# Kernel optimization log

Hardware: AMD Instinct MI355X
Metric: run time of the kernel (lower is better)

## Reference

```python
import jax, jax.numpy as jnp
import numpy as np

B, L, D, HD, DC = 2, 2048, 2048, 64, 2048
NH = D // HD  # 32 heads


def _rms_norm(x, eps):
    return x * jax.lax.rsqrt(jnp.mean(jnp.square(x), axis=-1, keepdims=True) + eps)


def _apply_rope(x, rope):
    # x: [b,h,l,d]; rope: [2,l,d]. x_hat = interleave(-x_odd, x_even)
    x2 = x.reshape(*x.shape[:-1], HD // 2, 2)
    x_hat = jnp.stack([-x2[..., 1], x2[..., 0]], axis=-1).reshape(x.shape)
    return x * rope[0] + x_hat * rope[1]


def setup_inputs() -> dict:
    key = jax.random.key(0)
    ks = jax.random.split(key, 6)
    return {
        "x": jax.random.normal(ks[0], (B, L, D), jnp.float32),
        "condition": jax.random.normal(ks[1], (B, DC), jnp.float32),
        "rope": jax.random.normal(ks[2], (2, L, HD), jnp.float32),
        "w_ada": jax.random.normal(ks[3], (2 * D, DC), jnp.float32) * 0.02,
        "w_qkv": jax.random.normal(ks[4], (3 * D, D), jnp.float32) * 0.02,
        "w_out": jax.random.normal(ks[5], (D, D), jnp.float32) * 0.02,
        "qk_w": jnp.ones((HD,), jnp.float32),
    }


def reference(x, condition, rope, w_ada, w_qkv, w_out, qk_w):
    eps = jnp.finfo(x.dtype).eps
    # AdaRMSNorm
    ss = (condition @ w_ada.T)[:, None, :]          # [b,1,2D]
    shift, scale = jnp.split(ss, 2, axis=-1)
    h = _rms_norm(x, eps) * (1.0 + scale) + shift   # [b,l,D]
    # fused QKV projection: 'b l (n h d)'
    qkv = (h @ w_qkv.T).reshape(B, L, 3, NH, HD)
    qkv = jnp.transpose(qkv, (2, 0, 3, 1, 4))       # [3,b,h,l,d]
    q, k, v = qkv[0], qkv[1], qkv[2]
    # per-head RMSNorm (with affine weight) + RoPE
    q = _apply_rope(_rms_norm(q, eps) * qk_w, rope)
    k = _apply_rope(_rms_norm(k, eps) * qk_w, rope)
    # SDPA
    scores = jnp.einsum('bhqd,bhkd->bhqk', q, k) / jnp.sqrt(jnp.asarray(HD, x.dtype))
    attn = jax.nn.softmax(scores, axis=-1)
    o = jnp.einsum('bhqk,bhkd->bhqd', attn, v)      # [b,h,l,d]
    o = jnp.transpose(o, (0, 2, 1, 3)).reshape(B, L, D)
    return o @ w_out.T
```

## Files before the change

### kernel.cpp

```cpp
#include <hip/hip_runtime.h>


typedef __bf16 bf16x8 __attribute__((ext_vector_type(8)));
typedef float  f32x4  __attribute__((ext_vector_type(4)));
typedef float  f32x16 __attribute__((ext_vector_type(16)));

#define EPS_F32 1.1920929e-07f
#define QSCALE 0.18033688011112042f

#if defined(__has_builtin)
#  if __has_builtin(__builtin_amdgcn_exp2f)
#    define EXP2F(x) __builtin_amdgcn_exp2f(x)
#  else
#    define EXP2F(x) __expf((x) * 0.6931471805599453f)
#  endif
#  if __has_builtin(__builtin_amdgcn_rcpf)
#    define RCPF(x) __builtin_amdgcn_rcpf(x)
#  else
#    define RCPF(x) (1.0f / (x))
#  endif
#else
#  define EXP2F(x) __expf((x) * 0.6931471805599453f)
#  define RCPF(x) (1.0f / (x))
#endif

__device__ __forceinline__ float bf2f(unsigned int u16) {
  union { unsigned int i; float f; } v; v.i = (u16 & 0xffffu) << 16; return v.f;
}
__device__ __forceinline__ float bf2f_hi(unsigned int u32) {
  union { unsigned int i; float f; } v; v.i = u32 & 0xffff0000u; return v.f;
}
__device__ __forceinline__ unsigned short f2bf(float f) {
  union { float f; unsigned int i; } v; v.f = f;
  unsigned int r = v.i + 0x7fffu + ((v.i >> 16) & 1u);
  return (unsigned short)(r >> 16);
}
__device__ __forceinline__ unsigned int f2bf_rn_u(float f) {
  union { float f; unsigned int i; } v; v.f = f;
  return v.i + 0x8000u;
}

__device__ __forceinline__ void gload16(const void* g, void* l) {
  __builtin_amdgcn_global_load_lds(
      (const __attribute__((address_space(1))) unsigned int*)(unsigned long long)g,
      (__attribute__((address_space(3))) unsigned int*)(unsigned int)(unsigned long long)l,
      16, 0, 0);
}

__global__ __launch_bounds__(256) void ada_gemm_kernel(
    const float* __restrict__ cond, const float* __restrict__ w_ada,
    float* __restrict__ ss)
{
  const int lane = threadIdx.x & 63;
  const int gw = blockIdx.x * 4 + (threadIdx.x >> 6);
  const int b = gw >> 12;
  const int j = gw & 4095;
  const float4* wr = (const float4*)(w_ada + j * 2048);
  const float4* cr = (const float4*)(cond + b * 2048);
  float acc = 0.f;
  #pragma unroll
  for (int k4 = 0; k4 < 8; ++k4) {
    float4 w = wr[lane + k4 * 64];
    float4 c = cr[lane + k4 * 64];
    acc += w.x * c.x + w.y * c.y + w.z * c.z + w.w * c.w;
  }
  #pragma unroll
  for (int off = 1; off < 64; off <<= 1) acc += __shfl_xor(acc, off);
  if (lane == 0) ss[b * 4096 + j] = acc;
}

__global__ __launch_bounds__(256) void ada_rms_kernel(
    const float* __restrict__ x, const float* __restrict__ ss,
    unsigned short* __restrict__ H)
{
  const int row = blockIdx.x;
  const int b = row >> 11;
  const int tid = threadIdx.x;
  const int lane = tid & 63, wave = tid >> 6;
  const float* xr = x + (size_t)row * 2048;
  float4 v0 = ((const float4*)xr)[tid * 2];
  float4 v1 = ((const float4*)xr)[tid * 2 + 1];
  float ssq = v0.x*v0.x + v0.y*v0.y + v0.z*v0.z + v0.w*v0.w
            + v1.x*v1.x + v1.y*v1.y + v1.z*v1.z + v1.w*v1.w;
  #pragma unroll
  for (int off = 1; off < 64; off <<= 1) ssq += __shfl_xor(ssq, off);
  __shared__ float red[4];
  if (lane == 0) red[wave] = ssq;
  __syncthreads();
  const float tot = red[0] + red[1] + red[2] + red[3];
  const float r = rsqrtf(tot * (1.f / 2048.f) + EPS_F32);
  const int c0 = tid * 8;
  const float* sh = ss + b * 4096;
  float xv[8] = {v0.x, v0.y, v0.z, v0.w, v1.x, v1.y, v1.z, v1.w};
  unsigned int pk[4];
  #pragma unroll
  for (int p = 0; p < 4; ++p) {
    const int c = c0 + p * 2;
    float h0 = xv[p*2+0] * r * (1.f + sh[2048 + c])     + sh[c];
    float h1 = xv[p*2+1] * r * (1.f + sh[2048 + c + 1]) + sh[c + 1];
    pk[p] = (unsigned int)f2bf(h0) | ((unsigned int)f2bf(h1) << 16);
  }
  *(uint4*)&H[(size_t)row * 2048 + c0] = make_uint4(pk[0], pk[1], pk[2], pk[3]);
}

__global__ __launch_bounds__(256) void cast2_kernel(
    const float* __restrict__ a,
    const float* __restrict__ b,
    unsigned short* __restrict__ dst)
{
  const int i = blockIdx.x * 256 + threadIdx.x;
  float4 v = (i < 3145728) ? ((const float4*)a)[i]
                           : ((const float4*)b)[i - 3145728];
  unsigned int p0 = (unsigned int)f2bf(v.x) | ((unsigned int)f2bf(v.y) << 16);
  unsigned int p1 = (unsigned int)f2bf(v.z) | ((unsigned int)f2bf(v.w) << 16);
  *(uint2*)&dst[(size_t)i * 4] = make_uint2(p0, p1);
}

__global__ __launch_bounds__(512, 2) void gemm_qkv_8p(
    const unsigned short* __restrict__ A,
    const unsigned short* __restrict__ Bw,
    unsigned short* __restrict__ C,
    unsigned short* __restrict__ vt)
{
  __shared__ unsigned short As[2][2][8192];
  __shared__ unsigned short Bs[2][2][8192];

  const int tid  = threadIdx.x;
  const int lane = tid & 63;
  const int wave = tid >> 6;
  const int wrow = (wave >> 2) * 128;
  const int wcol = (wave & 3) * 64;

  const int swz = (blockIdx.x & 7) * 48 + (blockIdx.x >> 3);
  const int bx = swz >> 4;
  const int by = swz & 15;
  const int bm = by * 256;
  const int bn = bx * 256;

  const int fr = lane & 15;
  const int q_ = lane >> 4;
  const int laneoff = fr * 32 + ((q_ ^ ((fr >> 1) & 3)) << 3);

  const int rA  = wave * 32 + (lane >> 2);
  const int kk  = (lane & 3) ^ ((lane >> 3) & 3);
  const unsigned short* Ag0 = A  + (size_t)(bm + rA) * 2048 + kk * 8;
  const unsigned short* Ag1 = Ag0 + (size_t)16 * 2048;
  const unsigned short* Bg0 = Bw + (size_t)(bn + rA) * 2048 + kk * 8;
  const unsigned short* Bg1 = Bg0 + (size_t)16 * 2048;
  const int ldso = rA * 32 + (lane & 3) * 8;

  f32x4 acc[8][4] = {};
  bf16x8 fA[4], fB[4];

#define STAGE_A(SB, SKH, KT) do { \
    gload16(Ag0 + (KT) * 64 + (SKH) * 32, &As[SB][SKH][ldso]); \
    gload16(Ag1 + (KT) * 64 + (SKH) * 32, &As[SB][SKH][ldso + 512]); } while (0)
#define STAGE_B(SB, SKH, KT) do { \
    gload16(Bg0 + (KT) * 64 + (SKH) * 32, &Bs[SB][SKH][ldso]); \
    gload16(Bg1 + (KT) * 64 + (SKH) * 32, &Bs[SB][SKH][ldso + 512]); } while (0)
#define VMW(N) asm volatile("s_waitcnt vmcnt(" #N ")" ::: "memory")
#define LDB(BUF, KH) do { const unsigned short* p_ = &Bs[BUF][KH][wcol * 32 + laneoff]; \
    fB[0] = *(const bf16x8*)&p_[0];    fB[1] = *(const bf16x8*)&p_[512]; \
    fB[2] = *(const bf16x8*)&p_[1024]; fB[3] = *(const bf16x8*)&p_[1536]; } while (0)
#define LDA(BUF, KH, MH) do { const unsigned short* p_ = &As[BUF][KH][(wrow + (MH) * 64) * 32 + laneoff]; \
    fA[0] = *(const bf16x8*)&p_[0];    fA[1] = *(const bf16x8*)&p_[512]; \
    fA[2] = *(const bf16x8*)&p_[1024]; fA[3] = *(const bf16x8*)&p_[1536]; } while (0)
#define MFMA16(MH) do { \
    _Pragma("unroll") \
    for (int f_ = 0; f_ < 4; ++f_) { \
      _Pragma("unroll") \
      for (int n_ = 0; n_ < 4; ++n_) \
        acc[(MH) * 4 + f_][n_] = __builtin_amdgcn_mfma_f32_16x16x32_bf16( \
            fA[f_], fB[n_], acc[(MH) * 4 + f_][n_], 0, 0, 0); \
    } } while (0)
#define PH_MID() do { __builtin_amdgcn_s_barrier(); \
    asm volatile("s_waitcnt lgkmcnt(0)"); \
    __builtin_amdgcn_s_setprio(1); } while (0)
#define PH_END() do { __builtin_amdgcn_s_setprio(0); \
    __builtin_amdgcn_s_barrier(); } while (0)

  STAGE_A(0, 0, 0); STAGE_B(0, 0, 0); STAGE_A(0, 1, 0); STAGE_B(0, 1, 0);
  VMW(4);
  __builtin_amdgcn_s_barrier();

  for (int it = 0; it < 16; ++it) {
    const int t1 = 2 * it + 1;
    const int t2 = 2 * it + 2;
    const bool pf = (it < 15);

    LDB(0, 0); LDA(0, 0, 0);
    STAGE_A(1, 0, t1);
    PH_MID(); MFMA16(0); PH_END();
    LDA(0, 0, 1);
    STAGE_B(1, 0, t1);
    VMW(4);
    PH_MID(); MFMA16(1); PH_END();
    LDB(0, 1); LDA(0, 1, 0);
    STAGE_A(1, 1, t1);
    PH_MID(); MFMA16(0); PH_END();
    LDA(0, 1, 1);
    STAGE_B(1, 1, t1);
    VMW(4);
    PH_MID(); MFMA16(1); PH_END();

    LDB(1, 0); LDA(1, 0, 0);
    if (pf) STAGE_A(0, 0, t2);
    PH_MID(); MFMA16(0); PH_END();
    LDA(1, 0, 1);
    if (pf) { STAGE_B(0, 0, t2); VMW(4); }
    else    { VMW(0); }
    PH_MID(); MFMA16(1); PH_END();
    LDB(1, 1); LDA(1, 1, 0);
    if (pf) STAGE_A(0, 1, t2);
    PH_MID(); MFMA16(0); PH_END();
    LDA(1, 1, 1);
    if (pf) STAGE_B(0, 1, t2);
    VMW(4);
    PH_MID(); MFMA16(1); PH_END();
  }

#undef STAGE_A
#undef STAGE_B
#undef VMW
#undef LDB
#undef LDA
#undef MFMA16
#undef PH_MID
#undef PH_END

  const int cr = (lane >> 4) * 4;
  const int cc = lane & 15;
  if (bn >= 4096) {
    #pragma unroll
    for (int mf = 0; mf < 8; ++mf)
      #pragma unroll
      for (int nf = 0; nf < 4; ++nf)
        #pragma unroll
        for (int r = 0; r < 4; ++r) {
          const int m  = bm + wrow + mf * 16 + cr + r;
          const int dg = bn + wcol + nf * 16 + cc - 4096;
          const int l  = m & 2047;
          const size_t dst = ((size_t)((m >> 11) * 32 + (dg >> 6)) * 64 + (dg & 63)) * 2048
                           + (l >> 6) * 64 + (l & 15) * 4 + ((l >> 4) & 3);
          vt[dst] = f2bf(acc[mf][nf][r]);
        }
  } else {
    #pragma unroll
    for (int mf = 0; mf < 8; ++mf)
      #pragma unroll
      for (int nf = 0; nf < 4; ++nf)
        #pragma unroll
        for (int r = 0; r < 4; ++r) {
          const int row = bm + wrow + mf * 16 + cr + r;
          const int col = bn + wcol + nf * 16 + cc;
          C[(size_t)row * 6144 + col] = f2bf(acc[mf][nf][r]);
        }
  }
}

__global__ __launch_bounds__(512, 1) void gemm_out_4p(
    const unsigned short* __restrict__ A,
    const unsigned short* __restrict__ Bw,
    float* __restrict__ C)
{
  __shared__ unsigned short As[2][2][8192];
  __shared__ unsigned short Bs[2][2][4096];

  const int tid  = threadIdx.x;
  const int lane = tid & 63;
  const int wave = tid >> 6;
  const int wrow = (wave >> 1) * 64;
  const int wcol = (wave & 1) * 64;

  const int swz = (blockIdx.x & 7) * 32 + (blockIdx.x >> 3);
  const int bx = swz >> 4;
  const int by = swz & 15;
  const int bm = by * 256;
  const int bn = bx * 128;

  const int fr = lane & 15;
  const int q_ = lane >> 4;
  const int laneoff = fr * 32 + ((q_ ^ ((fr >> 1) & 3)) << 3);

  const int rA = wave * 32 + (lane >> 2);
  const int rB = wave * 16 + (lane >> 2);
  const int kk = (lane & 3) ^ ((lane >> 3) & 3);
  const unsigned short* Ag0 = A  + (size_t)(bm + rA) * 2048 + kk * 8;
  const unsigned short* Ag1 = Ag0 + (size_t)16 * 2048;
  const unsigned short* Bg0 = Bw + (size_t)(bn + rB) * 2048 + kk * 8;
  const int ldsoA = rA * 32 + (lane & 3) * 8;
  const int ldsoB = rB * 32 + (lane & 3) * 8;

  f32x4 acc[4][4] = {};
  bf16x8 fA[4], fB[4];

#define STAGE_A4(SB, SKH, KT) do { \
    gload16(Ag0 + (KT) * 64 + (SKH) * 32, &As[SB][SKH][ldsoA]); \
    gload16(Ag1 + (KT) * 64 + (SKH) * 32, &As[SB][SKH][ldsoA + 512]); } while (0)
#define STAGE_B4(SB, SKH, KT) \
    gload16(Bg0 + (KT) * 64 + (SKH) * 32, &Bs[SB][SKH][ldsoB])
#define VMW(N) asm volatile("s_waitcnt vmcnt(" #N ")" ::: "memory")
#define LDB4(BUF, KH) do { const unsigned short* p_ = &Bs[BUF][KH][wcol * 32 + laneoff]; \
    fB[0] = *(const bf16x8*)&p_[0];    fB[1] = *(const bf16x8*)&p_[512]; \
    fB[2] = *(const bf16x8*)&p_[1024]; fB[3] = *(const bf16x8*)&p_[1536]; } while (0)
#define LDA4(BUF, KH) do { const unsigned short* p_ = &As[BUF][KH][wrow * 32 + laneoff]; \
    fA[0] = *(const bf16x8*)&p_[0];    fA[1] = *(const bf16x8*)&p_[512]; \
    fA[2] = *(const bf16x8*)&p_[1024]; fA[3] = *(const bf16x8*)&p_[1536]; } while (0)
#define MFMA16_4() do { \
    _Pragma("unroll") \
    for (int f_ = 0; f_ < 4; ++f_) { \
      _Pragma("unroll") \
      for (int n_ = 0; n_ < 4; ++n_) \
        acc[f_][n_] = __builtin_amdgcn_mfma_f32_16x16x32_bf16( \
            fA[f_], fB[n_], acc[f_][n_], 0, 0, 0); \
    } } while (0)
#define PH_MID() do { __builtin_amdgcn_s_barrier(); \
    asm volatile("s_waitcnt lgkmcnt(0)"); \
    __builtin_amdgcn_s_setprio(1); } while (0)
#define PH_END() do { __builtin_amdgcn_s_setprio(0); \
    __builtin_amdgcn_s_barrier(); } while (0)

  STAGE_A4(0, 0, 0); STAGE_B4(0, 0, 0);
  STAGE_A4(0, 1, 0); STAGE_B4(0, 1, 0);
  VMW(3);
  __builtin_amdgcn_s_barrier();

  for (int it = 0; it < 16; ++it) {
    const int t1 = 2 * it + 1;
    const int t2 = 2 * it + 2;
    const bool pf = (it < 15);

    LDB4(0, 0); LDA4(0, 0);
    STAGE_A4(1, 0, t1); STAGE_B4(1, 0, t1);
    VMW(3);
    PH_MID(); MFMA16_4(); PH_END();
    LDB4(0, 1); LDA4(0, 1);
    STAGE_A4(1, 1, t1); STAGE_B4(1, 1, t1);
    VMW(3);
    PH_MID(); MFMA16_4(); PH_END();

    LDB4(1, 0); LDA4(1, 0);
    if (pf) { STAGE_A4(0, 0, t2); STAGE_B4(0, 0, t2); VMW(3); }
    else    { VMW(0); }
    PH_MID(); MFMA16_4(); PH_END();
    LDB4(1, 1); LDA4(1, 1);
    if (pf) { STAGE_A4(0, 1, t2); STAGE_B4(0, 1, t2); VMW(3); }
    else    { VMW(0); }
    PH_MID(); MFMA16_4(); PH_END();
  }

#undef STAGE_A4
#undef STAGE_B4
#undef VMW
#undef LDB4
#undef LDA4
#undef MFMA16_4
#undef PH_MID
#undef PH_END

  const int cr = (lane >> 4) * 4;
  const int cc = lane & 15;
  #pragma unroll
  for (int f = 0; f < 4; ++f)
    #pragma unroll
    for (int n = 0; n < 4; ++n)
      #pragma unroll
      for (int r = 0; r < 4; ++r) {
        const int row = bm + wrow + f * 16 + cr + r;
        const int col = bn + wcol + n * 16 + cc;
        C[(size_t)row * 2048 + col] = acc[f][n][r];
      }
}

__global__ __launch_bounds__(256) void qk_rope_kernel(
    unsigned short* __restrict__ QKV, const float* __restrict__ rope,
    const float* __restrict__ qk_w)
{
  const int tid  = threadIdx.x;
  const int lane = tid & 63;
  const int task = blockIdx.x * 4 + (tid >> 6);
  const int hg   = task & 3;
  const int bl   = task >> 2;
  const int l    = bl & 2047;
  const int h    = hg * 8 + (lane >> 3);
  const int d0   = (lane & 7) * 8;
  const size_t base = (size_t)bl * 6144 + h * 64 + d0;

  float r0[8], r1[8], wv[8];
  {
    const float4* p0 = (const float4*)(rope + l * 64 + d0);
    const float4* p1 = (const float4*)(rope + 131072 + l * 64 + d0);
    const float4* pw = (const float4*)(qk_w + d0);
    float4 a, b2;
    a = p0[0]; b2 = p0[1];
    r0[0]=a.x; r0[1]=a.y; r0[2]=a.z; r0[3]=a.w; r0[4]=b2.x; r0[5]=b2.y; r0[6]=b2.z; r0[7]=b2.w;
    a = p1[0]; b2 = p1[1];
    r1[0]=a.x; r1[1]=a.y; r1[2]=a.z; r1[3]=a.w; r1[4]=b2.x; r1[5]=b2.y; r1[6]=b2.z; r1[7]=b2.w;
    a = pw[0]; b2 = pw[1];
    wv[0]=a.x; wv[1]=a.y; wv[2]=a.z; wv[3]=a.w; wv[4]=b2.x; wv[5]=b2.y; wv[6]=b2.z; wv[7]=b2.w;
  }

  #pragma unroll
  for (int t = 0; t < 2; ++t) {
    unsigned short* p = &QKV[base + (size_t)2048 * t];
    const uint4 raw = *(const uint4*)p;
    const unsigned int* u = (const unsigned int*)&raw;
    float v[8];
    #pragma unroll
    for (int j = 0; j < 4; ++j) {
      v[2*j]   = bf2f(u[j]);
      v[2*j+1] = bf2f_hi(u[j]);
    }
    float sq = v[0]*v[0] + v[1]*v[1] + v[2]*v[2] + v[3]*v[3]
             + v[4]*v[4] + v[5]*v[5] + v[6]*v[6] + v[7]*v[7];
    sq += __shfl_xor(sq, 1);
    sq += __shfl_xor(sq, 2);
    sq += __shfl_xor(sq, 4);
    const float rn = rsqrtf(sq * (1.f / 64.f) + EPS_F32)
                   * ((t == 0) ? QSCALE : 1.0f);
    float vn[8];
    #pragma unroll
    for (int j = 0; j < 8; ++j) vn[j] = v[j] * (rn * wv[j]);
    unsigned int pk[4];
    #pragma unroll
    for (int j = 0; j < 4; ++j) {
      const float o0 = vn[2*j]   * r0[2*j]   - vn[2*j+1] * r1[2*j];
      const float o1 = vn[2*j+1] * r0[2*j+1] + vn[2*j]   * r1[2*j+1];
      pk[j] = (unsigned int)f2bf(o0) | ((unsigned int)f2bf(o1) << 16);
    }
    *(uint4*)p = make_uint4(pk[0], pk[1], pk[2], pk[3]);
  }
}

__global__ __launch_bounds__(256, 2) void attn_mfma_kernel(
    const unsigned short* __restrict__ QKV,
    const unsigned short* __restrict__ Vt,
    unsigned short* __restrict__ O)
{
  __shared__ unsigned short Ks[64 * 72];
  __shared__ unsigned short Vs[64 * 72];
  __shared__ unsigned short Ps[4 * 64 * 68];
  const int tid  = threadIdx.x;
  const int lane = tid & 63;
  const int wave = tid >> 6;
  const int blk = blockIdx.x;
  const int bh = blk & 63;
  const int qt = blk >> 6;
  const int b = bh >> 5, h = bh & 31;
  const int rowbase = b << 11;
  const int qbase = qt * 256 + wave * 64;

  const int m16  = lane & 15;
  const int quad = lane >> 4;
  const int m32  = lane & 31;
  const int hl   = lane >> 5;

  bf16x8 qf[4][2];
  #pragma unroll
  for (int qi = 0; qi < 4; ++qi)
    #pragma unroll
    for (int ch = 0; ch < 2; ++ch)
      qf[qi][ch] = *(const bf16x8*)&QKV[(size_t)(rowbase + qbase + qi * 16 + m16) * 6144
                                        + h * 64 + ch * 32 + quad * 8];

  const int sr = tid >> 2;
  const int sc = (tid & 3) * 16;
  const unsigned short* Kg = QKV + (size_t)(rowbase + sr) * 6144 + 2048 + h * 64 + sc;
  const unsigned short* Vg = Vt + (size_t)(bh * 64 + sr) * 2048 + sc;

  f32x16 accO[2][2] = {};
  float part[4][4] = {};
  unsigned short* Pw = &Ps[(wave * 64) * 68];

  for (int kt = 0; kt < 32; ++kt) {
    __syncthreads();
    {
      const uint4* kp = (const uint4*)(Kg + (size_t)kt * 64 * 6144);
      const uint4* vp = (const uint4*)(Vg + kt * 64);
      uint4 k0 = kp[0], k1 = kp[1];
      uint4 v0 = vp[0], v1 = vp[1];
      *(uint4*)&Ks[sr * 72 + sc]     = k0;
      *(uint4*)&Ks[sr * 72 + sc + 8] = k1;
      *(uint4*)&Vs[sr * 72 + sc]     = v0;
      *(uint4*)&Vs[sr * 72 + sc + 8] = v1;
    }
    __syncthreads();

    unsigned int pk[4][4][2];
    #pragma unroll
    for (int kj = 0; kj < 4; ++kj) {
      bf16x8 kf0 = *(const bf16x8*)&Ks[(kj * 16 + m16) * 72 + quad * 8];
      bf16x8 kf1 = *(const bf16x8*)&Ks[(kj * 16 + m16) * 72 + 32 + quad * 8];
      #pragma unroll
      for (int qi = 0; qi < 4; ++qi) {
        f32x4 acc = {};
        acc = __builtin_amdgcn_mfma_f32_16x16x32_bf16(qf[qi][0], kf0, acc, 0, 0, 0);
        acc = __builtin_amdgcn_mfma_f32_16x16x32_bf16(qf[qi][1], kf1, acc, 0, 0, 0);
        #pragma unroll
        for (int r = 0; r < 4; ++r) {
          float p = EXP2F(acc[r]);
          part[qi][r] += p;
          unsigned int pb = f2bf_rn_u(p);
          if (kj == 0)      pk[qi][r][0]  = pb >> 16;
          else if (kj == 1) pk[qi][r][0] |= pb & 0xffff0000u;
          else if (kj == 2) pk[qi][r][1]  = pb >> 16;
          else              pk[qi][r][1] |= pb & 0xffff0000u;
        }
      }
    }
    #pragma unroll
    for (int qi = 0; qi < 4; ++qi)
      #pragma unroll
      for (int r = 0; r < 4; ++r)
        *(uint2*)&Pw[(qi * 16 + quad * 4 + r) * 68 + m16 * 4] =
            make_uint2(pk[qi][r][0], pk[qi][r][1]);

    #pragma unroll
    for (int ch = 0; ch < 4; ++ch) {
      bf16x8 pa0 = *(const bf16x8*)&Pw[m32 * 68 + ch * 16 + hl * 8];
      bf16x8 pa1 = *(const bf16x8*)&Pw[(32 + m32) * 68 + ch * 16 + hl * 8];
      bf16x8 vb0 = *(const bf16x8*)&Vs[m32 * 72 + ch * 16 + hl * 8];
      bf16x8 vb1 = *(const bf16x8*)&Vs[(32 + m32) * 72 + ch * 16 + hl * 8];
      accO[0][0] = __builtin_amdgcn_mfma_f32_32x32x16_bf16(pa0, vb0, accO[0][0], 0, 0, 0);
      accO[0][1] = __builtin_amdgcn_mfma_f32_32x32x16_bf16(pa0, vb1, accO[0][1], 0, 0, 0);
      accO[1][0] = __builtin_amdgcn_mfma_f32_32x32x16_bf16(pa1, vb0, accO[1][0], 0, 0, 0);
      accO[1][1] = __builtin_amdgcn_mfma_f32_32x32x16_bf16(pa1, vb1, accO[1][1], 0, 0, 0);
    }
  }

  #pragma unroll
  for (int qi = 0; qi < 4; ++qi)
    #pragma unroll
    for (int r = 0; r < 4; ++r)
      #pragma unroll
      for (int off = 1; off < 16; off <<= 1)
        part[qi][r] += __shfl_xor(part[qi][r], off);

  #pragma unroll
  for (int qs = 0; qs < 2; ++qs) {
    #pragma unroll
    for (int reg = 0; reg < 16; ++reg) {
      const int r = reg & 3;
      const int s = reg >> 2;
      const int qsrc = ((2 * s + hl) & 3) * 16 + m16;
      const float rs = __shfl(part[qs * 2 + (reg >> 3)][r], qsrc);
      const float inv = RCPF(rs);
      const int rho = r + 8 * s + 4 * hl;
      const size_t base = (size_t)(rowbase + qbase + qs * 32 + rho) * 2048 + h * 64;
      O[base + m32]      = f2bf(accO[qs][0][reg] * inv);
      O[base + 32 + m32] = f2bf(accO[qs][1][reg] * inv);
    }
  }
}

extern "C" void kernel_launch(void* const* d_in, const int* in_sizes, int n_in,
                              void* d_out, int out_size, void* d_ws, size_t ws_size,
                              hipStream_t stream) {
  (void)in_sizes; (void)n_in; (void)out_size; (void)ws_size;
  const float* x     = (const float*)d_in[0];
  const float* cond  = (const float*)d_in[1];
  const float* rope  = (const float*)d_in[2];
  const float* w_ada = (const float*)d_in[3];
  const float* w_qkv = (const float*)d_in[4];
  const float* w_out = (const float*)d_in[5];
  const float* qk_w  = (const float*)d_in[6];
  float* out = (float*)d_out;

  char* ws = (char*)d_ws;
  float*          ss   = (float*)ws;
  unsigned short* H    = (unsigned short*)(ws + 32768);
  unsigned short* Wq   = H + 8388608;
  unsigned short* Wo   = Wq + 12582912;
  unsigned short* QKV  = Wo + 4194304;
  unsigned short* Vt_g = QKV + 25165824;

  ada_gemm_kernel<<<2048, 256, 0, stream>>>(cond, w_ada, ss);
  ada_rms_kernel<<<4096, 256, 0, stream>>>(x, ss, H);
  cast2_kernel<<<16384, 256, 0, stream>>>(w_qkv, w_out, Wq);
  gemm_qkv_8p<<<384, 512, 0, stream>>>(H, Wq, QKV, Vt_g);
  qk_rope_kernel<<<4096, 256, 0, stream>>>(QKV, rope, qk_w);
  attn_mfma_kernel<<<512, 256, 0, stream>>>(QKV, Vt_g, H);
  gemm_out_4p<<<256, 512, 0, stream>>>(H, Wo, out);
}
```

Before: 432.7 us.

## Fuse weight cast into ada prep kernel and split QKV GEMM into QK and V

```diff
diff --git a/kernel.cpp b/kernel.cpp
--- a/kernel.cpp
+++ b/kernel.cpp
@@ -47,10 +47,21 @@
       16, 0, 0);
 }
 
-__global__ __launch_bounds__(256) void ada_gemm_kernel(
+__global__ __launch_bounds__(256) void prep_kernel(
     const float* __restrict__ cond, const float* __restrict__ w_ada,
-    float* __restrict__ ss)
+    float* __restrict__ ss,
+    const float* __restrict__ wq_f, const float* __restrict__ wo_f,
+    unsigned short* __restrict__ dst)
 {
+  if (blockIdx.x >= 2048) {
+    const int i = (blockIdx.x - 2048) * 256 + threadIdx.x;
+    float4 v = (i < 3145728) ? ((const float4*)wq_f)[i]
+                             : ((const float4*)wo_f)[i - 3145728];
+    unsigned int p0 = (unsigned int)f2bf(v.x) | ((unsigned int)f2bf(v.y) << 16);
+    unsigned int p1 = (unsigned int)f2bf(v.z) | ((unsigned int)f2bf(v.w) << 16);
+    *(uint2*)&dst[(size_t)i * 4] = make_uint2(p0, p1);
+    return;
+  }
   const int lane = threadIdx.x & 63;
   const int gw = blockIdx.x * 4 + (threadIdx.x >> 6);
   const int b = gw >> 12;
@@ -103,24 +114,10 @@
   *(uint4*)&H[(size_t)row * 2048 + c0] = make_uint4(pk[0], pk[1], pk[2], pk[3]);
 }
 
-__global__ __launch_bounds__(256) void cast2_kernel(
-    const float* __restrict__ a,
-    const float* __restrict__ b,
-    unsigned short* __restrict__ dst)
-{
-  const int i = blockIdx.x * 256 + threadIdx.x;
-  float4 v = (i < 3145728) ? ((const float4*)a)[i]
-                           : ((const float4*)b)[i - 3145728];
-  unsigned int p0 = (unsigned int)f2bf(v.x) | ((unsigned int)f2bf(v.y) << 16);
-  unsigned int p1 = (unsigned int)f2bf(v.z) | ((unsigned int)f2bf(v.w) << 16);
-  *(uint2*)&dst[(size_t)i * 4] = make_uint2(p0, p1);
-}
-
-__global__ __launch_bounds__(512, 2) void gemm_qkv_8p(
+__global__ __launch_bounds__(512, 2) void gemm_qk_8p(
     const unsigned short* __restrict__ A,
     const unsigned short* __restrict__ Bw,
-    unsigned short* __restrict__ C,
-    unsigned short* __restrict__ vt)
+    unsigned short* __restrict__ C)
 {
   __shared__ unsigned short As[2][2][8192];
   __shared__ unsigned short Bs[2][2][8192];
@@ -131,7 +128,7 @@
   const int wrow = (wave >> 2) * 128;
   const int wcol = (wave & 3) * 64;
 
-  const int swz = (blockIdx.x & 7) * 48 + (blockIdx.x >> 3);
+  const int swz = (blockIdx.x & 7) * 32 + (blockIdx.x >> 3);
   const int bx = swz >> 4;
   const int by = swz & 15;
   const int bm = by * 256;
@@ -230,38 +227,22 @@
 
   const int cr = (lane >> 4) * 4;
   const int cc = lane & 15;
-  if (bn >= 4096) {
-    #pragma unroll
-    for (int mf = 0; mf < 8; ++mf)
+  #pragma unroll
+  for (int mf = 0; mf < 8; ++mf)
+    #pragma unroll
+    for (int nf = 0; nf < 4; ++nf)
       #pragma unroll
-      for (int nf = 0; nf < 4; ++nf)
-        #pragma unroll
-        for (int r = 0; r < 4; ++r) {
-          const int m  = bm + wrow + mf * 16 + cr + r;
-          const int dg = bn + wcol + nf * 16 + cc - 4096;
-          const int l  = m & 2047;
-          const size_t dst = ((size_t)((m >> 11) * 32 + (dg >> 6)) * 64 + (dg & 63)) * 2048
-                           + (l >> 6) * 64 + (l & 15) * 4 + ((l >> 4) & 3);
-          vt[dst] = f2bf(acc[mf][nf][r]);
-        }
-  } else {
-    #pragma unroll
-    for (int mf = 0; mf < 8; ++mf)
-      #pragma unroll
-      for (int nf = 0; nf < 4; ++nf)
-        #pragma unroll
-        for (int r = 0; r < 4; ++r) {
-          const int row = bm + wrow + mf * 16 + cr + r;
-          const int col = bn + wcol + nf * 16 + cc;
-          C[(size_t)row * 6144 + col] = f2bf(acc[mf][nf][r]);
-        }
-  }
-}
-
-__global__ __launch_bounds__(512, 1) void gemm_out_4p(
+      for (int r = 0; r < 4; ++r) {
+        const int row = bm + wrow + mf * 16 + cr + r;
+        const int col = bn + wcol + nf * 16 + cc;
+        C[(size_t)row * 6144 + col] = f2bf(acc[mf][nf][r]);
+      }
+}
+
+__global__ __launch_bounds__(512, 1) void gemm_v_4p(
     const unsigned short* __restrict__ A,
     const unsigned short* __restrict__ Bw,
-    float* __restrict__ C)
+    unsigned short* __restrict__ vt)
 {
   __shared__ unsigned short As[2][2][8192];
   __shared__ unsigned short Bs[2][2][4096];
@@ -366,6 +347,123 @@
     for (int n = 0; n < 4; ++n)
       #pragma unroll
       for (int r = 0; r < 4; ++r) {
+        const int m  = bm + wrow + f * 16 + cr + r;
+        const int dg = bn + wcol + n * 16 + cc;
+        const int l  = m & 2047;
+        const size_t dst = ((size_t)((m >> 11) * 32 + (dg >> 6)) * 64 + (dg & 63)) * 2048
+                         + (l >> 6) * 64 + (l & 15) * 4 + ((l >> 4) & 3);
+        vt[dst] = f2bf(acc[f][n][r]);
+      }
+}
+
+__global__ __launch_bounds__(512, 1) void gemm_out_4p(
+    const unsigned short* __restrict__ A,
+    const unsigned short* __restrict__ Bw,
+    float* __restrict__ C)
+{
+  __shared__ unsigned short As[2][2][8192];
+  __shared__ unsigned short Bs[2][2][4096];
+
+  const int tid  = threadIdx.x;
+  const int lane = tid & 63;
+  const int wave = tid >> 6;
+  const int wrow = (wave >> 1) * 64;
+  const int wcol = (wave & 1) * 64;
+
+  const int swz = (blockIdx.x & 7) * 32 + (blockIdx.x >> 3);
+  const int bx = swz >> 4;
+  const int by = swz & 15;
+  const int bm = by * 256;
+  const int bn = bx * 128;
+
+  const int fr = lane & 15;
+  const int q_ = lane >> 4;
+  const int laneoff = fr * 32 + ((q_ ^ ((fr >> 1) & 3)) << 3);
+
+  const int rA = wave * 32 + (lane >> 2);
+  const int rB = wave * 16 + (lane >> 2);
+  const int kk = (lane & 3) ^ ((lane >> 3) & 3);
+  const unsigned short* Ag0 = A  + (size_t)(bm + rA) * 2048 + kk * 8;
+  const unsigned short* Ag1 = Ag0 + (size_t)16 * 2048;
+  const unsigned short* Bg0 = Bw + (size_t)(bn + rB) * 2048 + kk * 8;
+  const int ldsoA = rA * 32 + (lane & 3) * 8;
+  const int ldsoB = rB * 32 + (lane & 3) * 8;
+
+  f32x4 acc[4][4] = {};
+  bf16x8 fA[4], fB[4];
+
+#define STAGE_A4(SB, SKH, KT) do { \
+    gload16(Ag0 + (KT) * 64 + (SKH) * 32, &As[SB][SKH][ldsoA]); \
+    gload16(Ag1 + (KT) * 64 + (SKH) * 32, &As[SB][SKH][ldsoA + 512]); } while (0)
+#define STAGE_B4(SB, SKH, KT) \
+    gload16(Bg0 + (KT) * 64 + (SKH) * 32, &Bs[SB][SKH][ldsoB])
+#define VMW(N) asm volatile("s_waitcnt vmcnt(" #N ")" ::: "memory")
+#define LDB4(BUF, KH) do { const unsigned short* p_ = &Bs[BUF][KH][wcol * 32 + laneoff]; \
+    fB[0] = *(const bf16x8*)&p_[0];    fB[1] = *(const bf16x8*)&p_[512]; \
+    fB[2] = *(const bf16x8*)&p_[1024]; fB[3] = *(const bf16x8*)&p_[1536]; } while (0)
+#define LDA4(BUF, KH) do { const unsigned short* p_ = &As[BUF][KH][wrow * 32 + laneoff]; \
+    fA[0] = *(const bf16x8*)&p_[0];    fA[1] = *(const bf16x8*)&p_[512]; \
+    fA[2] = *(const bf16x8*)&p_[1024]; fA[3] = *(const bf16x8*)&p_[1536]; } while (0)
+#define MFMA16_4() do { \
+    _Pragma("unroll") \
+    for (int f_ = 0; f_ < 4; ++f_) { \
+      _Pragma("unroll") \
+      for (int n_ = 0; n_ < 4; ++n_) \
+        acc[f_][n_] = __builtin_amdgcn_mfma_f32_16x16x32_bf16( \
+            fA[f_], fB[n_], acc[f_][n_], 0, 0, 0); \
+    } } while (0)
+#define PH_MID() do { __builtin_amdgcn_s_barrier(); \
+    asm volatile("s_waitcnt lgkmcnt(0)"); \
+    __builtin_amdgcn_s_setprio(1); } while (0)
+#define PH_END() do { __builtin_amdgcn_s_setprio(0); \
+    __builtin_amdgcn_s_barrier(); } while (0)
+
+  STAGE_A4(0, 0, 0); STAGE_B4(0, 0, 0);
+  STAGE_A4(0, 1, 0); STAGE_B4(0, 1, 0);
+  VMW(3);
+  __builtin_amdgcn_s_barrier();
+
+  for (int it = 0; it < 16; ++it) {
+    const int t1 = 2 * it + 1;
+    const int t2 = 2 * it + 2;
+    const bool pf = (it < 15);
+
+    LDB4(0, 0); LDA4(0, 0);
+    STAGE_A4(1, 0, t1); STAGE_B4(1, 0, t1);
+    VMW(3);
+    PH_MID(); MFMA16_4(); PH_END();
+    LDB4(0, 1); LDA4(0, 1);
+    STAGE_A4(1, 1, t1); STAGE_B4(1, 1, t1);
+    VMW(3);
+    PH_MID(); MFMA16_4(); PH_END();
+
+    LDB4(1, 0); LDA4(1, 0);
+    if (pf) { STAGE_A4(0, 0, t2); STAGE_B4(0, 0, t2); VMW(3); }
+    else    { VMW(0); }
+    PH_MID(); MFMA16_4(); PH_END();
+    LDB4(1, 1); LDA4(1, 1);
+    if (pf) { STAGE_A4(0, 1, t2); STAGE_B4(0, 1, t2); VMW(3); }
+    else    { VMW(0); }
+    PH_MID(); MFMA16_4(); PH_END();
+  }
+
+#undef STAGE_A4
+#undef STAGE_B4
+#undef VMW
+#undef LDB4
+#undef LDA4
+#undef MFMA16_4
+#undef PH_MID
+#undef PH_END
+
+  const int cr = (lane >> 4) * 4;
+  const int cc = lane & 15;
+  #pragma unroll
+  for (int f = 0; f < 4; ++f)
+    #pragma unroll
+    for (int n = 0; n < 4; ++n)
+      #pragma unroll
+      for (int r = 0; r < 4; ++r) {
         const int row = bm + wrow + f * 16 + cr + r;
         const int col = bn + wcol + n * 16 + cc;
         C[(size_t)row * 2048 + col] = acc[f][n][r];
@@ -574,10 +672,10 @@
   unsigned short* QKV  = Wo + 4194304;
   unsigned short* Vt_g = QKV + 25165824;
 
-  ada_gemm_kernel<<<2048, 256, 0, stream>>>(cond, w_ada, ss);
+  prep_kernel<<<18432, 256, 0, stream>>>(cond, w_ada, ss, w_qkv, w_out, Wq);
   ada_rms_kernel<<<4096, 256, 0, stream>>>(x, ss, H);
-  cast2_kernel<<<16384, 256, 0, stream>>>(w_qkv, w_out, Wq);
-  gemm_qkv_8p<<<384, 512, 0, stream>>>(H, Wq, QKV, Vt_g);
+  gemm_qk_8p<<<256, 512, 0, stream>>>(H, Wq, QKV);
+  gemm_v_4p<<<256, 512, 0, stream>>>(H, Wq + (size_t)4096 * 2048, Vt_g);
   qk_rope_kernel<<<4096, 256, 0, stream>>>(QKV, rope, qk_w);
   attn_mfma_kernel<<<512, 256, 0, stream>>>(QKV, Vt_g, H);
   gemm_out_4p<<<256, 512, 0, stream>>>(H, Wo, out);
```

After: 442.7 us. 1.02x slower.
